# Kernel optimization log

Measured on AMD Instinct MI355X. Metric: run time of the kernel, lower is better.

Reference implementation:

```python
import jax, jax.numpy as jnp
import numpy as np

HEADS = 4
BN_EPS = 1e-5


def _linear_attention(x, heads):
    # x: [B, L, C]; per-head linear attention: softmax(Q,dim=feat) @ (softmax(K,dim=seq)^T @ V)
    B, L, C = x.shape
    dh = C // heads
    h = x.reshape(B, L, heads, dh)
    q = jax.nn.softmax(h, axis=-1)          # softmax over feature dim (dim=2 in torch)
    k = jax.nn.softmax(h, axis=1)           # softmax over sequence dim (dim=1 in torch)
    kv = jnp.einsum('blhd,blhe->bhde', k, h)   # [B, H, dh, dh]
    out = jnp.einsum('blhd,bhde->blhe', q, kv) # [B, L, H, dh]
    return out.reshape(B, L, C)


def setup_inputs() -> dict:
    key = jax.random.key(0)
    ks = jax.random.split(key, 10)
    B, C, L, DOUT, NB = 32, 32, 16384, 10, 3
    s = 0.1
    return {
        'x': jax.random.normal(ks[0], (B, C, L), jnp.float32),
        'fcW1': jax.random.normal(ks[1], (NB, C, C), jnp.float32) * s,
        'fcb1': jax.random.normal(ks[2], (NB, C), jnp.float32) * s,
        'fcW2': jax.random.normal(ks[3], (NB, C, C), jnp.float32) * s,
        'fcb2': jax.random.normal(ks[4], (NB, C), jnp.float32) * s,
        'Wh': jax.random.normal(ks[5], (C, C), jnp.float32) * s,
        'bh': jax.random.normal(ks[6], (C,), jnp.float32) * s,
        'bn_gamma': jnp.ones((C,), jnp.float32),
        'bn_beta': jnp.zeros((C,), jnp.float32),
        'bn_mean': jnp.zeros((C,), jnp.float32),
        'bn_var': jnp.ones((C,), jnp.float32),
        'Wf': jax.random.normal(ks[7], (C, DOUT), jnp.float32) * s,
        'bf': jax.random.normal(ks[8], (DOUT,), jnp.float32) * s,
    }


def reference(x, fcW1, fcb1, fcW2, fcb2, Wh, bh, bn_gamma, bn_beta, bn_mean, bn_var, Wf, bf):
    gelu = lambda t: jax.nn.gelu(t, approximate=False)  # torch default GELU is exact erf
    h = jnp.transpose(x, (0, 2, 1))  # [B, C, L] -> [B, L, C]
    n_blocks = fcW1.shape[0]
    for i in range(n_blocks):
        h = _linear_attention(h, HEADS)
        h = gelu(h @ fcW1[i] + fcb1[i])
        h = gelu(h @ fcW2[i] + fcb2[i])
    pooled = jnp.mean(h, axis=1)  # AdaptiveAvgPool1d(1) over L -> [B, C]
    y = pooled @ Wh + bh
    y = (y - bn_mean) * jax.lax.rsqrt(bn_var + BN_EPS) * bn_gamma + bn_beta  # BatchNorm1d (eval)
    y = gelu(y)
    return y @ Wf + bf
```

## Files before the change

### kernel.cpp

```cpp
#include <hip/hip_runtime.h>
#include <cstddef>

#define B_ 32
#define C_ 32
#define L_ 16384
#define H_ 4
#define DH_ 8
#define NB_ 3
#define DOUT_ 10
#define SEG_ 512
#define S_ (L_/SEG_)

#define TILE 256
#define AST  40
#define OST  260

typedef _Float16 f16_t;
typedef _Float16 f16x2 __attribute__((ext_vector_type(2)));
typedef _Float16 f16x8 __attribute__((ext_vector_type(8)));
typedef float    f32x4 __attribute__((ext_vector_type(4)));

__device__ __forceinline__ float gelu_f(float x){
    const float z  = fabsf(x) * 0.70710678118654752440f;
    const float t  = __builtin_amdgcn_rcpf(fmaf(0.3275911f, z, 1.0f));
    const float e  = __expf(-z * z);
    float p = fmaf(t, 1.061405429f, -1.453152027f);
    p = fmaf(t, p, 1.421413741f);
    p = fmaf(t, p, -0.284496736f);
    p = fmaf(t, p, 0.254829592f);
    const float erfz = 1.0f - p * t * e;
    const float phi  = fmaf(copysignf(erfz, x), 0.5f, 0.5f);
    return x * phi;
}

__global__ __launch_bounds__(256) void stats_kernel(const float* __restrict__ h,
                                                    float* __restrict__ part){
    const int seg = blockIdx.x;
    const int hd  = blockIdx.y;
    const int b   = blockIdx.z;
    const int t   = threadIdx.x;
    const int d   = t >> 5;
    const int j   = t & 31;

    __shared__ float tile[8][SEG_];
    __shared__ float sm[8];

    const float* hb = h + (size_t)b * ((size_t)C_*L_) + (size_t)(hd*DH_)*L_ + (size_t)seg*SEG_;

    for (int f = t; f < 8*SEG_/4; f += 256){
        const int row = f >> 7;
        const int c4  = (f & 127) << 2;
        *(f32x4*)&tile[row][c4] = *(const f32x4*)&hb[(size_t)row*L_ + c4];
    }
    __syncthreads();

    float m = -INFINITY;
    #pragma unroll
    for (int i = 0; i < SEG_/32; i++) m = fmaxf(m, tile[d][j + 32*i]);
    m = fmaxf(m, __shfl_xor(m, 1));
    m = fmaxf(m, __shfl_xor(m, 2));
    m = fmaxf(m, __shfl_xor(m, 4));
    m = fmaxf(m, __shfl_xor(m, 8));
    m = fmaxf(m, __shfl_xor(m, 16));
    if (j == 0) sm[d] = m;
    const float m_d = m;

    float s = 0.0f;
    float kv[8];
    #pragma unroll
    for (int e = 0; e < 8; e++) kv[e] = 0.0f;
    #pragma unroll
    for (int i = 0; i < SEG_/32; i++){
        const int k = j + 32*i;
        const float ek = __expf(tile[d][k] - m_d);
        s += ek;
        #pragma unroll
        for (int e = 0; e < 8; e++) kv[e] = fmaf(ek, tile[e][k], kv[e]);
    }
    s += __shfl_xor(s, 1);  s += __shfl_xor(s, 2);  s += __shfl_xor(s, 4);
    s += __shfl_xor(s, 8);  s += __shfl_xor(s, 16);
    #pragma unroll
    for (int e = 0; e < 8; e++){
        kv[e] += __shfl_xor(kv[e], 1);  kv[e] += __shfl_xor(kv[e], 2);
        kv[e] += __shfl_xor(kv[e], 4);  kv[e] += __shfl_xor(kv[e], 8);
        kv[e] += __shfl_xor(kv[e], 16);
    }
    __syncthreads();

    float* po = part + (size_t)((b*H_ + hd)*S_ + seg) * 80;
    if (j == 0){
        po[8 + d] = s;
        #pragma unroll
        for (int e = 0; e < 8; e++) po[16 + d*8 + e] = kv[e];
    }
    if (t < 8) po[t] = sm[t];
}

__global__ __launch_bounds__(64) void merge_kernel(const float* __restrict__ part,
                                                   float* __restrict__ kvn){
    const int bh = blockIdx.x;
    const int t  = threadIdx.x;
    const int d  = t >> 3;
    const float* p = part + (size_t)bh * S_ * 80;
    float M = -INFINITY;
    for (int s2 = 0; s2 < S_; s2++) M = fmaxf(M, p[s2*80 + d]);
    float ssum = 0.0f, kvsum = 0.0f;
    for (int s2 = 0; s2 < S_; s2++){
        float sc = __expf(p[s2*80 + d] - M);
        ssum  += p[s2*80 + 8  + d] * sc;
        kvsum += p[s2*80 + 16 + t] * sc;
    }
    kvn[(size_t)bh*64 + t] = kvsum / ssum;
}

template<bool LAST>
__global__ __launch_bounds__(256)
__attribute__((amdgpu_waves_per_eu(3, 4)))
void block_kernel(const float* hin,
                  float* hout,
                  const float* __restrict__ kvn,
                  const float* __restrict__ W1,
                  const float* __restrict__ b1,
                  const float* __restrict__ W2,
                  const float* __restrict__ b2,
                  float* __restrict__ pooled){
    __shared__ f16_t Ash[TILE*AST];
    __shared__ f16_t Bsh1[32*AST];
    __shared__ f16_t Bsh2[32*AST];
    __shared__ float sb1[32], sb2[32];
    __shared__ float O16[16*OST];
    __shared__ float pool[32];

    const int tid = threadIdx.x;
    const int b   = blockIdx.y;
    const int l0  = blockIdx.x * TILE;
    const int l   = l0 + tid;
    const size_t base = (size_t)b * ((size_t)C_*L_);
    const float* kv = kvn + (size_t)b * (H_*DH_*DH_);

    for (int i = tid; i < 1024; i += 256){
        const int k = i >> 5, n = i & 31;
        Bsh1[n*AST + k] = (f16_t)W1[i];
        Bsh2[n*AST + k] = (f16_t)W2[i];
    }
    if (tid < 32){ sb1[tid] = b1[tid]; sb2[tid] = b2[tid]; }
    if (LAST && tid < 32) pool[tid] = 0.0f;

    float h[32];
    #pragma unroll
    for (int c = 0; c < 32; c++) h[c] = hin[base + (size_t)c*L_ + l];

    float attn[32];
    #pragma unroll
    for (int hh = 0; hh < 4; hh++){
        float mq = h[hh*8];
        #pragma unroll
        for (int d2 = 1; d2 < 8; d2++) mq = fmaxf(mq, h[hh*8 + d2]);
        float es[8]; float qs = 0.f;
        #pragma unroll
        for (int d2 = 0; d2 < 8; d2++){ es[d2] = __expf(h[hh*8 + d2] - mq); qs += es[d2]; }
        const float inv = __builtin_amdgcn_rcpf(qs);
        #pragma unroll
        for (int e = 0; e < 8; e++){
            float a = 0.f;
            #pragma unroll
            for (int d2 = 0; d2 < 8; d2++) a += es[d2] * kv[hh*64 + d2*8 + e];
            attn[hh*8 + e] = a * inv;
        }
    }

    #pragma unroll
    for (int k2 = 0; k2 < 32; k2 += 2){
        f16x2 pr = { (f16_t)attn[k2], (f16_t)attn[k2+1] };
        *(f16x2*)&Ash[tid*AST + k2] = pr;
    }
    __syncthreads();

    const int wv   = tid >> 6;
    const int lane = tid & 63;
    const int lr   = lane & 15;
    const int lk   = lane >> 4;
    const f32x4 zero = {0.f, 0.f, 0.f, 0.f};

    f16x8 a[4], bw[2];
    f32x4 d[8];

    #pragma unroll
    for (int mt = 0; mt < 4; mt++)
        a[mt] = *(const f16x8*)&Ash[(wv*64 + mt*16 + lr)*AST + lk*8];
    #pragma unroll
    for (int nt = 0; nt < 2; nt++)
        bw[nt] = *(const f16x8*)&Bsh1[(nt*16 + lr)*AST + lk*8];
    #pragma unroll
    for (int nt = 0; nt < 2; nt++)
        #pragma unroll
        for (int mt = 0; mt < 4; mt++)
            d[nt*4+mt] = __builtin_amdgcn_mfma_f32_16x16x32_f16(a[mt], bw[nt], zero, 0, 0, 0);

    #pragma unroll
    for (int nt = 0; nt < 2; nt++){
        const float bias = sb1[nt*16 + lr];
        #pragma unroll
        for (int mt = 0; mt < 4; mt++){
            #pragma unroll
            for (int r = 0; r < 4; r++){
                const float v = gelu_f(d[nt*4+mt][r] + bias);
                Ash[(wv*64 + mt*16 + lk*4 + r)*AST + (nt*16 + lr)] = (f16_t)v;
            }
        }
    }
    __syncthreads();

    #pragma unroll
    for (int mt = 0; mt < 4; mt++)
        a[mt] = *(const f16x8*)&Ash[(wv*64 + mt*16 + lr)*AST + lk*8];
    #pragma unroll
    for (int nt = 0; nt < 2; nt++)
        bw[nt] = *(const f16x8*)&Bsh2[(nt*16 + lr)*AST + lk*8];
    #pragma unroll
    for (int nt = 0; nt < 2; nt++)
        #pragma unroll
        for (int mt = 0; mt < 4; mt++)
            d[nt*4+mt] = __builtin_amdgcn_mfma_f32_16x16x32_f16(a[mt], bw[nt], zero, 0, 0, 0);

    #pragma unroll
    for (int nt = 0; nt < 2; nt++){
        const float bias = sb2[nt*16 + lr];
        #pragma unroll
        for (int mt = 0; mt < 4; mt++)
            #pragma unroll
            for (int r = 0; r < 4; r++)
                d[nt*4+mt][r] = gelu_f(d[nt*4+mt][r] + bias);
    }

    if (!LAST){
        #pragma unroll
        for (int nt = 0; nt < 2; nt++){
            __syncthreads();
            #pragma unroll
            for (int mt = 0; mt < 4; mt++)
                *(f32x4*)&O16[lr*OST + wv*64 + mt*16 + lk*4] = d[nt*4+mt];
            __syncthreads();
            #pragma unroll
            for (int c = 0; c < 16; c++)
                hout[base + (size_t)(nt*16 + c)*L_ + l0 + tid] = O16[c*OST + tid];
        }
    } else {
        __syncthreads();
        #pragma unroll
        for (int nt = 0; nt < 2; nt++){
            float ps = 0.f;
            #pragma unroll
            for (int mt = 0; mt < 4; mt++)
                ps += d[nt*4+mt][0] + d[nt*4+mt][1] + d[nt*4+mt][2] + d[nt*4+mt][3];
            atomicAdd(&pool[nt*16 + lr], ps);
        }
        __syncthreads();
        if (tid < 32) atomicAdd(&pooled[b*32 + tid], pool[tid]);
    }
}

__global__ __launch_bounds__(1024) void head_kernel(const float* __restrict__ pooled,
                                                    const float* __restrict__ Wh,
                                                    const float* __restrict__ bh,
                                                    const float* __restrict__ gam,
                                                    const float* __restrict__ bet,
                                                    const float* __restrict__ mean,
                                                    const float* __restrict__ var,
                                                    const float* __restrict__ Wf,
                                                    const float* __restrict__ bf,
                                                    float* __restrict__ out){
    __shared__ float y2[32][32];
    const int t = threadIdx.x;
    const int b = t >> 5, c = t & 31;
    float a = bh[c];
    const float invL = 1.0f / (float)L_;
    #pragma unroll
    for (int d = 0; d < 32; d++) a += (pooled[b*32 + d] * invL) * Wh[d*32 + c];
    a = (a - mean[c]) * rsqrtf(var[c] + 1e-5f) * gam[c] + bet[c];
    y2[b][c] = gelu_f(a);
    __syncthreads();
    if (t < B_*DOUT_){
        const int b2 = t / DOUT_, j = t % DOUT_;
        float r = bf[j];
        #pragma unroll
        for (int c2 = 0; c2 < 32; c2++) r += y2[b2][c2] * Wf[c2*DOUT_ + j];
        out[t] = r;
    }
}

extern "C" void kernel_launch(void* const* d_in, const int* in_sizes, int n_in,
                              void* d_out, int out_size, void* d_ws, size_t ws_size,
                              hipStream_t stream){
    (void)in_sizes; (void)n_in; (void)out_size; (void)ws_size;
    const float* x    = (const float*)d_in[0];
    const float* fW1  = (const float*)d_in[1];
    const float* fb1  = (const float*)d_in[2];
    const float* fW2  = (const float*)d_in[3];
    const float* fb2  = (const float*)d_in[4];
    const float* Wh   = (const float*)d_in[5];
    const float* bh   = (const float*)d_in[6];
    const float* gam  = (const float*)d_in[7];
    const float* bet  = (const float*)d_in[8];
    const float* mean = (const float*)d_in[9];
    const float* var  = (const float*)d_in[10];
    const float* Wf   = (const float*)d_in[11];
    const float* bf   = (const float*)d_in[12];
    float* out = (float*)d_out;

    float* hbuf   = (float*)d_ws;
    float* part   = hbuf + (size_t)B_*C_*L_;
    float* kvn    = part + (size_t)B_*H_*S_*80;
    float* pooled = kvn  + (size_t)B_*H_*64;

    hipMemsetAsync(pooled, 0, B_*C_*sizeof(float), stream);

    dim3 sgrid(S_, H_, B_);
    dim3 bgrid(L_/TILE, B_);

    stats_kernel<<<sgrid, 256, 0, stream>>>(x, part);
    merge_kernel<<<B_*H_, 64, 0, stream>>>(part, kvn);
    block_kernel<false><<<bgrid, 256, 0, stream>>>(x, hbuf, kvn, fW1, fb1, fW2, fb2, nullptr);
    stats_kernel<<<sgrid, 256, 0, stream>>>(hbuf, part);
    merge_kernel<<<B_*H_, 64, 0, stream>>>(part, kvn);
    block_kernel<false><<<bgrid, 256, 0, stream>>>(hbuf, hbuf, kvn,
        fW1 + C_*C_, fb1 + C_, fW2 + C_*C_, fb2 + C_, nullptr);
    stats_kernel<<<sgrid, 256, 0, stream>>>(hbuf, part);
    merge_kernel<<<B_*H_, 64, 0, stream>>>(part, kvn);
    block_kernel<true><<<bgrid, 256, 0, stream>>>(hbuf, nullptr, kvn,
        fW1 + 2*C_*C_, fb1 + 2*C_, fW2 + 2*C_*C_, fb2 + 2*C_, pooled);

    head_kernel<<<1, 1024, 0, stream>>>(pooled, Wh, bh, gam, bet, mean, var, Wf, bf, out);
}
```

Before: 289.0 us.

## Fuse next-block attention stats into block kernel epilogue and parallelize merge

The block kernel now computes the per-tile softmax max, sum and K^T V partials for the next block while the output tile is still in shared memory. This removes two separate stats_kernel passes that re-read the full activation buffer from global memory. The merge kernel uses 256 threads with a shared-memory reduction over a configurable segment count. Shared memory is reduced by aliasing the A and O staging buffers, and the occupancy hint is raised. The trade-offs are more partial segments to merge, extra register pressure in the epilogue, and a risk of aliasing bugs between the A and O buffers.

After: 311.7 us. 1.08x slower.

```diff
diff --git a/kernel.cpp b/kernel.cpp
--- a/kernel.cpp
+++ b/kernel.cpp
@@ -10,6 +10,7 @@
 #define DOUT_ 10
 #define SEG_ 512
 #define S_ (L_/SEG_)
+#define S2_ (L_/256)
 
 #define TILE 256
 #define AST  40
@@ -33,6 +34,13 @@
     return x * phi;
 }
 
+#define RED_MAX32(v) do{ v = fmaxf(v, __shfl_xor(v,1));  v = fmaxf(v, __shfl_xor(v,2)); \
+                         v = fmaxf(v, __shfl_xor(v,4));  v = fmaxf(v, __shfl_xor(v,8)); \
+                         v = fmaxf(v, __shfl_xor(v,16)); }while(0)
+#define RED_SUM32(v) do{ v += __shfl_xor(v,1);  v += __shfl_xor(v,2); \
+                         v += __shfl_xor(v,4);  v += __shfl_xor(v,8); \
+                         v += __shfl_xor(v,16); }while(0)
+
 __global__ __launch_bounds__(256) void stats_kernel(const float* __restrict__ h,
                                                     float* __restrict__ part){
     const int seg = blockIdx.x;
@@ -57,11 +65,7 @@
     float m = -INFINITY;
     #pragma unroll
     for (int i = 0; i < SEG_/32; i++) m = fmaxf(m, tile[d][j + 32*i]);
-    m = fmaxf(m, __shfl_xor(m, 1));
-    m = fmaxf(m, __shfl_xor(m, 2));
-    m = fmaxf(m, __shfl_xor(m, 4));
-    m = fmaxf(m, __shfl_xor(m, 8));
-    m = fmaxf(m, __shfl_xor(m, 16));
+    RED_MAX32(m);
     if (j == 0) sm[d] = m;
     const float m_d = m;
 
@@ -77,14 +81,9 @@
         #pragma unroll
         for (int e = 0; e < 8; e++) kv[e] = fmaf(ek, tile[e][k], kv[e]);
     }
-    s += __shfl_xor(s, 1);  s += __shfl_xor(s, 2);  s += __shfl_xor(s, 4);
-    s += __shfl_xor(s, 8);  s += __shfl_xor(s, 16);
-    #pragma unroll
-    for (int e = 0; e < 8; e++){
-        kv[e] += __shfl_xor(kv[e], 1);  kv[e] += __shfl_xor(kv[e], 2);
-        kv[e] += __shfl_xor(kv[e], 4);  kv[e] += __shfl_xor(kv[e], 8);
-        kv[e] += __shfl_xor(kv[e], 16);
-    }
+    RED_SUM32(s);
+    #pragma unroll
+    for (int e = 0; e < 8; e++){ RED_SUM32(kv[e]); }
     __syncthreads();
 
     float* po = part + (size_t)((b*H_ + hd)*S_ + seg) * 80;
@@ -96,26 +95,41 @@
     if (t < 8) po[t] = sm[t];
 }
 
-__global__ __launch_bounds__(64) void merge_kernel(const float* __restrict__ part,
-                                                   float* __restrict__ kvn){
+__global__ __launch_bounds__(256) void merge_kernel(const float* __restrict__ part,
+                                                    float* __restrict__ kvn,
+                                                    int nseg){
     const int bh = blockIdx.x;
-    const int t  = threadIdx.x;
+    const int t  = threadIdx.x & 63;
+    const int g  = threadIdx.x >> 6;
     const int d  = t >> 3;
-    const float* p = part + (size_t)bh * S_ * 80;
+    const float* p = part + (size_t)bh * nseg * 80;
+    __shared__ float r1[4][64], r2[4][64];
+
     float M = -INFINITY;
-    for (int s2 = 0; s2 < S_; s2++) M = fmaxf(M, p[s2*80 + d]);
+    for (int s2 = g; s2 < nseg; s2 += 4) M = fmaxf(M, p[s2*80 + d]);
+    r1[g][t] = M;
+    __syncthreads();
+    M = fmaxf(fmaxf(r1[0][t], r1[1][t]), fmaxf(r1[2][t], r1[3][t]));
+    __syncthreads();
+
     float ssum = 0.0f, kvsum = 0.0f;
-    for (int s2 = 0; s2 < S_; s2++){
-        float sc = __expf(p[s2*80 + d] - M);
+    for (int s2 = g; s2 < nseg; s2 += 4){
+        const float sc = __expf(p[s2*80 + d] - M);
         ssum  += p[s2*80 + 8  + d] * sc;
         kvsum += p[s2*80 + 16 + t] * sc;
     }
-    kvn[(size_t)bh*64 + t] = kvsum / ssum;
-}
-
-template<bool LAST>
+    r1[g][t] = ssum; r2[g][t] = kvsum;
+    __syncthreads();
+    if (g == 0){
+        ssum  = r1[0][t]+r1[1][t]+r1[2][t]+r1[3][t];
+        kvsum = r2[0][t]+r2[1][t]+r2[2][t]+r2[3][t];
+        kvn[(size_t)bh*64 + t] = kvsum / ssum;
+    }
+}
+
+template<bool LAST, bool STATS>
 __global__ __launch_bounds__(256)
-__attribute__((amdgpu_waves_per_eu(3, 4)))
+__attribute__((amdgpu_waves_per_eu(6, 8)))
 void block_kernel(const float* hin,
                   float* hout,
                   const float* __restrict__ kvn,
@@ -123,12 +137,14 @@
                   const float* __restrict__ b1,
                   const float* __restrict__ W2,
                   const float* __restrict__ b2,
-                  float* __restrict__ pooled){
-    __shared__ f16_t Ash[TILE*AST];
+                  float* __restrict__ pooled,
+                  float* __restrict__ partout){
+    __shared__ __align__(16) char AObuf[TILE*AST*2];
+    f16_t* const Ash = (f16_t*)AObuf;
+    float* const O16 = (float*)AObuf;
     __shared__ f16_t Bsh1[32*AST];
     __shared__ f16_t Bsh2[32*AST];
     __shared__ float sb1[32], sb2[32];
-    __shared__ float O16[16*OST];
     __shared__ float pool[32];
 
     const int tid = threadIdx.x;
@@ -244,6 +260,43 @@
             #pragma unroll
             for (int c = 0; c < 16; c++)
                 hout[base + (size_t)(nt*16 + c)*L_ + l0 + tid] = O16[c*OST + tid];
+
+            if constexpr (STATS){
+                const int sd = tid >> 5;
+                const int sj = tid & 31;
+                #pragma unroll
+                for (int hh2 = 0; hh2 < 2; hh2++){
+                    const int row = hh2*8 + sd;
+                    float m = -INFINITY;
+                    #pragma unroll
+                    for (int i = 0; i < 8; i++) m = fmaxf(m, O16[row*OST + sj + 32*i]);
+                    RED_MAX32(m);
+                    float s = 0.0f;
+                    float kvp[8];
+                    #pragma unroll
+                    for (int e = 0; e < 8; e++) kvp[e] = 0.0f;
+                    #pragma unroll
+                    for (int i = 0; i < 8; i++){
+                        const int k = sj + 32*i;
+                        const float ek = __expf(O16[row*OST + k] - m);
+                        s += ek;
+                        #pragma unroll
+                        for (int e = 0; e < 8; e++)
+                            kvp[e] = fmaf(ek, O16[(hh2*8+e)*OST + k], kvp[e]);
+                    }
+                    RED_SUM32(s);
+                    #pragma unroll
+                    for (int e = 0; e < 8; e++){ RED_SUM32(kvp[e]); }
+                    if (sj == 0){
+                        float* po = partout +
+                            (size_t)((b*H_ + nt*2 + hh2)*S2_ + blockIdx.x) * 80;
+                        po[sd]     = m;
+                        po[8 + sd] = s;
+                        #pragma unroll
+                        for (int e = 0; e < 8; e++) po[16 + sd*8 + e] = kvp[e];
+                    }
+                }
+            }
         }
     } else {
         __syncthreads();
@@ -310,7 +363,7 @@
 
     float* hbuf   = (float*)d_ws;
     float* part   = hbuf + (size_t)B_*C_*L_;
-    float* kvn    = part + (size_t)B_*H_*S_*80;
+    float* kvn    = part + (size_t)B_*H_*S2_*80;
     float* pooled = kvn  + (size_t)B_*H_*64;
 
     hipMemsetAsync(pooled, 0, B_*C_*sizeof(float), stream);
@@ -319,16 +372,15 @@
     dim3 bgrid(L_/TILE, B_);
 
     stats_kernel<<<sgrid, 256, 0, stream>>>(x, part);
-    merge_kernel<<<B_*H_, 64, 0, stream>>>(part, kvn);
-    block_kernel<false><<<bgrid, 256, 0, stream>>>(x, hbuf, kvn, fW1, fb1, fW2, fb2, nullptr);
-    stats_kernel<<<sgrid, 256, 0, stream>>>(hbuf, part);
-    merge_kernel<<<B_*H_, 64, 0, stream>>>(part, kvn);
-    block_kernel<false><<<bgrid, 256, 0, stream>>>(hbuf, hbuf, kvn,
-        fW1 + C_*C_, fb1 + C_, fW2 + C_*C_, fb2 + C_, nullptr);
-    stats_kernel<<<sgrid, 256, 0, stream>>>(hbuf, part);
-    merge_kernel<<<B_*H_, 64, 0, stream>>>(part, kvn);
-    block_kernel<true><<<bgrid, 256, 0, stream>>>(hbuf, nullptr, kvn,
-        fW1 + 2*C_*C_, fb1 + 2*C_, fW2 + 2*C_*C_, fb2 + 2*C_, pooled);
+    merge_kernel<<<B_*H_, 256, 0, stream>>>(part, kvn, S_);
+    block_kernel<false, true><<<bgrid, 256, 0, stream>>>(x, hbuf, kvn,
+        fW1, fb1, fW2, fb2, nullptr, part);
+    merge_kernel<<<B_*H_, 256, 0, stream>>>(part, kvn, S2_);
+    block_kernel<false, true><<<bgrid, 256, 0, stream>>>(hbuf, hbuf, kvn,
+        fW1 + C_*C_, fb1 + C_, fW2 + C_*C_, fb2 + C_, nullptr, part);
+    merge_kernel<<<B_*H_, 256, 0, stream>>>(part, kvn, S2_);
+    block_kernel<true, false><<<bgrid, 256, 0, stream>>>(hbuf, nullptr, kvn,
+        fW1 + 2*C_*C_, fb1 + 2*C_, fW2 + 2*C_*C_, fb2 + 2*C_, pooled, nullptr);
 
     head_kernel<<<1, 1024, 0, stream>>>(pooled, Wh, bh, gam, bet, mean, var, Wf, bf, out);
 }
```

## Fuse segment-merge into block kernel and alias A/O shared buffers

Applied to the files above, without the earlier changes.

Removes the separate merge kernel: each block now recomputes the per-(batch,head) normalized KV matrix from the per-segment partials directly into shared memory. This eliminates three small kernel launches and the kvn round-trip, at the cost of redundant merge work in every block (64 blocks per batch each read 32 segments of partials). The activation loads are hoisted earlier to overlap with the merge, and the f16 A tile and f32 output staging buffer now share one LDS allocation to cut shared-memory use and potentially raise occupancy.

Measured after the change: 294.1 us. No clear change (+1.7%).

```diff
diff --git a/kernel.cpp b/kernel.cpp
--- a/kernel.cpp
+++ b/kernel.cpp
@@ -33,6 +33,13 @@
     return x * phi;
 }
 
+#define RED_MAX32(v) do{ v = fmaxf(v, __shfl_xor(v,1));  v = fmaxf(v, __shfl_xor(v,2)); \
+                         v = fmaxf(v, __shfl_xor(v,4));  v = fmaxf(v, __shfl_xor(v,8)); \
+                         v = fmaxf(v, __shfl_xor(v,16)); }while(0)
+#define RED_SUM32(v) do{ v += __shfl_xor(v,1);  v += __shfl_xor(v,2); \
+                         v += __shfl_xor(v,4);  v += __shfl_xor(v,8); \
+                         v += __shfl_xor(v,16); }while(0)
+
 __global__ __launch_bounds__(256) void stats_kernel(const float* __restrict__ h,
                                                     float* __restrict__ part){
     const int seg = blockIdx.x;
@@ -57,11 +64,7 @@
     float m = -INFINITY;
     #pragma unroll
     for (int i = 0; i < SEG_/32; i++) m = fmaxf(m, tile[d][j + 32*i]);
-    m = fmaxf(m, __shfl_xor(m, 1));
-    m = fmaxf(m, __shfl_xor(m, 2));
-    m = fmaxf(m, __shfl_xor(m, 4));
-    m = fmaxf(m, __shfl_xor(m, 8));
-    m = fmaxf(m, __shfl_xor(m, 16));
+    RED_MAX32(m);
     if (j == 0) sm[d] = m;
     const float m_d = m;
 
@@ -77,14 +80,9 @@
         #pragma unroll
         for (int e = 0; e < 8; e++) kv[e] = fmaf(ek, tile[e][k], kv[e]);
     }
-    s += __shfl_xor(s, 1);  s += __shfl_xor(s, 2);  s += __shfl_xor(s, 4);
-    s += __shfl_xor(s, 8);  s += __shfl_xor(s, 16);
-    #pragma unroll
-    for (int e = 0; e < 8; e++){
-        kv[e] += __shfl_xor(kv[e], 1);  kv[e] += __shfl_xor(kv[e], 2);
-        kv[e] += __shfl_xor(kv[e], 4);  kv[e] += __shfl_xor(kv[e], 8);
-        kv[e] += __shfl_xor(kv[e], 16);
-    }
+    RED_SUM32(s);
+    #pragma unroll
+    for (int e = 0; e < 8; e++){ RED_SUM32(kv[e]); }
     __syncthreads();
 
     float* po = part + (size_t)((b*H_ + hd)*S_ + seg) * 80;
@@ -94,23 +92,6 @@
         for (int e = 0; e < 8; e++) po[16 + d*8 + e] = kv[e];
     }
     if (t < 8) po[t] = sm[t];
-}
-
-__global__ __launch_bounds__(64) void merge_kernel(const float* __restrict__ part,
-                                                   float* __restrict__ kvn){
-    const int bh = blockIdx.x;
-    const int t  = threadIdx.x;
-    const int d  = t >> 3;
-    const float* p = part + (size_t)bh * S_ * 80;
-    float M = -INFINITY;
-    for (int s2 = 0; s2 < S_; s2++) M = fmaxf(M, p[s2*80 + d]);
-    float ssum = 0.0f, kvsum = 0.0f;
-    for (int s2 = 0; s2 < S_; s2++){
-        float sc = __expf(p[s2*80 + d] - M);
-        ssum  += p[s2*80 + 8  + d] * sc;
-        kvsum += p[s2*80 + 16 + t] * sc;
-    }
-    kvn[(size_t)bh*64 + t] = kvsum / ssum;
 }
 
 template<bool LAST>
@@ -118,17 +99,19 @@
 __attribute__((amdgpu_waves_per_eu(3, 4)))
 void block_kernel(const float* hin,
                   float* hout,
-                  const float* __restrict__ kvn,
+                  const float* __restrict__ part,
                   const float* __restrict__ W1,
                   const float* __restrict__ b1,
                   const float* __restrict__ W2,
                   const float* __restrict__ b2,
                   float* __restrict__ pooled){
-    __shared__ f16_t Ash[TILE*AST];
+    __shared__ __align__(16) char AObuf[TILE*AST*2];
+    f16_t* const Ash = (f16_t*)AObuf;
+    float* const O16 = (float*)AObuf;
     __shared__ f16_t Bsh1[32*AST];
     __shared__ f16_t Bsh2[32*AST];
     __shared__ float sb1[32], sb2[32];
-    __shared__ float O16[16*OST];
+    __shared__ float kvsh[256];
     __shared__ float pool[32];
 
     const int tid = threadIdx.x;
@@ -136,7 +119,10 @@
     const int l0  = blockIdx.x * TILE;
     const int l   = l0 + tid;
     const size_t base = (size_t)b * ((size_t)C_*L_);
-    const float* kv = kvn + (size_t)b * (H_*DH_*DH_);
+
+    float h[32];
+    #pragma unroll
+    for (int c = 0; c < 32; c++) h[c] = hin[base + (size_t)c*L_ + l];
 
     for (int i = tid; i < 1024; i += 256){
         const int k = i >> 5, n = i & 31;
@@ -146,9 +132,22 @@
     if (tid < 32){ sb1[tid] = b1[tid]; sb2[tid] = b2[tid]; }
     if (LAST && tid < 32) pool[tid] = 0.0f;
 
-    float h[32];
-    #pragma unroll
-    for (int c = 0; c < 32; c++) h[c] = hin[base + (size_t)c*L_ + l];
+    {
+        const int hh_t = tid >> 6;
+        const int tt   = tid & 63;
+        const int dd   = tt >> 3;
+        const float* pp = part + (size_t)(b*H_ + hh_t) * S_ * 80;
+        float M = -INFINITY;
+        for (int s2 = 0; s2 < S_; s2++) M = fmaxf(M, pp[s2*80 + dd]);
+        float ssum = 0.0f, kvs = 0.0f;
+        for (int s2 = 0; s2 < S_; s2++){
+            const float sc = __expf(pp[s2*80 + dd] - M);
+            ssum = fmaf(pp[s2*80 + 8  + dd], sc, ssum);
+            kvs  = fmaf(pp[s2*80 + 16 + tt], sc, kvs);
+        }
+        kvsh[tid] = kvs / ssum;
+    }
+    __syncthreads();
 
     float attn[32];
     #pragma unroll
@@ -164,7 +163,7 @@
         for (int e = 0; e < 8; e++){
             float a = 0.f;
             #pragma unroll
-            for (int d2 = 0; d2 < 8; d2++) a += es[d2] * kv[hh*64 + d2*8 + e];
+            for (int d2 = 0; d2 < 8; d2++) a += es[d2] * kvsh[hh*64 + d2*8 + e];
             attn[hh*8 + e] = a * inv;
         }
     }
@@ -310,8 +309,7 @@
 
     float* hbuf   = (float*)d_ws;
     float* part   = hbuf + (size_t)B_*C_*L_;
-    float* kvn    = part + (size_t)B_*H_*S_*80;
-    float* pooled = kvn  + (size_t)B_*H_*64;
+    float* pooled = part + (size_t)B_*H_*S_*80;
 
     hipMemsetAsync(pooled, 0, B_*C_*sizeof(float), stream);
 
@@ -319,15 +317,13 @@
     dim3 bgrid(L_/TILE, B_);
 
     stats_kernel<<<sgrid, 256, 0, stream>>>(x, part);
-    merge_kernel<<<B_*H_, 64, 0, stream>>>(part, kvn);
-    block_kernel<false><<<bgrid, 256, 0, stream>>>(x, hbuf, kvn, fW1, fb1, fW2, fb2, nullptr);
+    block_kernel<false><<<bgrid, 256, 0, stream>>>(x, hbuf, part,
+        fW1, fb1, fW2, fb2, nullptr);
     stats_kernel<<<sgrid, 256, 0, stream>>>(hbuf, part);
-    merge_kernel<<<B_*H_, 64, 0, stream>>>(part, kvn);
-    block_kernel<false><<<bgrid, 256, 0, stream>>>(hbuf, hbuf, kvn,
+    block_kernel<false><<<bgrid, 256, 0, stream>>>(hbuf, hbuf, part,
         fW1 + C_*C_, fb1 + C_, fW2 + C_*C_, fb2 + C_, nullptr);
     stats_kernel<<<sgrid, 256, 0, stream>>>(hbuf, part);
-    merge_kernel<<<B_*H_, 64, 0, stream>>>(part, kvn);
-    block_kernel<true><<<bgrid, 256, 0, stream>>>(hbuf, nullptr, kvn,
+    block_kernel<true><<<bgrid, 256, 0, stream>>>(hbuf, nullptr, part,
         fW1 + 2*C_*C_, fb1 + 2*C_, fW2 + 2*C_*C_, fb2 + 2*C_, pooled);
 
     head_kernel<<<1, 1024, 0, stream>>>(pooled, Wh, bh, gam, bet, mean, var, Wf, bf, out);
```

## Store block outputs directly from MFMA registers and parallelize merge kernel

Applied to the files above, without the earlier changes.

The non-last block kernel now writes MFMA results straight to global memory as 16-byte vector stores. This drops the shared-memory transpose buffer and its barriers, and removes the barrier after the first GELU because each wave only reads back its own rows of Ash. The merge kernel uses 256 threads, with four groups each covering a quarter of the segments, and combines them through shared memory. The activation loads are moved ahead of weight staging so they are issued earlier. The cost is less coalesced stores: each row receives scattered 64-byte chunks instead of full contiguous rows, which may raise write traffic inefficiency, in exchange for lower LDS use and fewer synchronizations.

After: 298.2 us. 3.2% more time.

```diff
diff --git a/kernel.cpp b/kernel.cpp
--- a/kernel.cpp
+++ b/kernel.cpp
@@ -13,7 +13,6 @@
 
 #define TILE 256
 #define AST  40
-#define OST  260
 
 typedef _Float16 f16_t;
 typedef _Float16 f16x2 __attribute__((ext_vector_type(2)));
@@ -33,6 +32,13 @@
     return x * phi;
 }
 
+#define RED_MAX32(v) do{ v = fmaxf(v, __shfl_xor(v,1));  v = fmaxf(v, __shfl_xor(v,2)); \
+                         v = fmaxf(v, __shfl_xor(v,4));  v = fmaxf(v, __shfl_xor(v,8)); \
+                         v = fmaxf(v, __shfl_xor(v,16)); }while(0)
+#define RED_SUM32(v) do{ v += __shfl_xor(v,1);  v += __shfl_xor(v,2); \
+                         v += __shfl_xor(v,4);  v += __shfl_xor(v,8); \
+                         v += __shfl_xor(v,16); }while(0)
+
 __global__ __launch_bounds__(256) void stats_kernel(const float* __restrict__ h,
                                                     float* __restrict__ part){
     const int seg = blockIdx.x;
@@ -57,11 +63,7 @@
     float m = -INFINITY;
     #pragma unroll
     for (int i = 0; i < SEG_/32; i++) m = fmaxf(m, tile[d][j + 32*i]);
-    m = fmaxf(m, __shfl_xor(m, 1));
-    m = fmaxf(m, __shfl_xor(m, 2));
-    m = fmaxf(m, __shfl_xor(m, 4));
-    m = fmaxf(m, __shfl_xor(m, 8));
-    m = fmaxf(m, __shfl_xor(m, 16));
+    RED_MAX32(m);
     if (j == 0) sm[d] = m;
     const float m_d = m;
 
@@ -77,14 +79,9 @@
         #pragma unroll
         for (int e = 0; e < 8; e++) kv[e] = fmaf(ek, tile[e][k], kv[e]);
     }
-    s += __shfl_xor(s, 1);  s += __shfl_xor(s, 2);  s += __shfl_xor(s, 4);
-    s += __shfl_xor(s, 8);  s += __shfl_xor(s, 16);
-    #pragma unroll
-    for (int e = 0; e < 8; e++){
-        kv[e] += __shfl_xor(kv[e], 1);  kv[e] += __shfl_xor(kv[e], 2);
-        kv[e] += __shfl_xor(kv[e], 4);  kv[e] += __shfl_xor(kv[e], 8);
-        kv[e] += __shfl_xor(kv[e], 16);
-    }
+    RED_SUM32(s);
+    #pragma unroll
+    for (int e = 0; e < 8; e++){ RED_SUM32(kv[e]); }
     __syncthreads();
 
     float* po = part + (size_t)((b*H_ + hd)*S_ + seg) * 80;
@@ -96,21 +93,35 @@
     if (t < 8) po[t] = sm[t];
 }
 
-__global__ __launch_bounds__(64) void merge_kernel(const float* __restrict__ part,
-                                                   float* __restrict__ kvn){
+__global__ __launch_bounds__(256) void merge_kernel(const float* __restrict__ part,
+                                                    float* __restrict__ kvn){
     const int bh = blockIdx.x;
-    const int t  = threadIdx.x;
+    const int t  = threadIdx.x & 63;
+    const int g  = threadIdx.x >> 6;
     const int d  = t >> 3;
     const float* p = part + (size_t)bh * S_ * 80;
+    __shared__ float r1[4][64], r2[4][64];
+
     float M = -INFINITY;
-    for (int s2 = 0; s2 < S_; s2++) M = fmaxf(M, p[s2*80 + d]);
+    for (int s2 = g; s2 < S_; s2 += 4) M = fmaxf(M, p[s2*80 + d]);
+    r1[g][t] = M;
+    __syncthreads();
+    M = fmaxf(fmaxf(r1[0][t], r1[1][t]), fmaxf(r1[2][t], r1[3][t]));
+    __syncthreads();
+
     float ssum = 0.0f, kvsum = 0.0f;
-    for (int s2 = 0; s2 < S_; s2++){
-        float sc = __expf(p[s2*80 + d] - M);
+    for (int s2 = g; s2 < S_; s2 += 4){
+        const float sc = __expf(p[s2*80 + d] - M);
         ssum  += p[s2*80 + 8  + d] * sc;
         kvsum += p[s2*80 + 16 + t] * sc;
     }
-    kvn[(size_t)bh*64 + t] = kvsum / ssum;
+    r1[g][t] = ssum; r2[g][t] = kvsum;
+    __syncthreads();
+    if (g == 0){
+        ssum  = r1[0][t]+r1[1][t]+r1[2][t]+r1[3][t];
+        kvsum = r2[0][t]+r2[1][t]+r2[2][t]+r2[3][t];
+        kvn[(size_t)bh*64 + t] = kvsum / ssum;
+    }
 }
 
 template<bool LAST>
@@ -124,11 +135,10 @@
                   const float* __restrict__ W2,
                   const float* __restrict__ b2,
                   float* __restrict__ pooled){
-    __shared__ f16_t Ash[TILE*AST];
+    __shared__ __align__(16) f16_t Ash[TILE*AST];
     __shared__ f16_t Bsh1[32*AST];
     __shared__ f16_t Bsh2[32*AST];
     __shared__ float sb1[32], sb2[32];
-    __shared__ float O16[16*OST];
     __shared__ float pool[32];
 
     const int tid = threadIdx.x;
@@ -138,6 +148,10 @@
     const size_t base = (size_t)b * ((size_t)C_*L_);
     const float* kv = kvn + (size_t)b * (H_*DH_*DH_);
 
+    float h[32];
+    #pragma unroll
+    for (int c = 0; c < 32; c++) h[c] = hin[base + (size_t)c*L_ + l];
+
     for (int i = tid; i < 1024; i += 256){
         const int k = i >> 5, n = i & 31;
         Bsh1[n*AST + k] = (f16_t)W1[i];
@@ -145,10 +159,6 @@
     }
     if (tid < 32){ sb1[tid] = b1[tid]; sb2[tid] = b2[tid]; }
     if (LAST && tid < 32) pool[tid] = 0.0f;
-
-    float h[32];
-    #pragma unroll
-    for (int c = 0; c < 32; c++) h[c] = hin[base + (size_t)c*L_ + l];
 
     float attn[32];
     #pragma unroll
@@ -201,15 +211,13 @@
     for (int nt = 0; nt < 2; nt++){
         const float bias = sb1[nt*16 + lr];
         #pragma unroll
-        for (int mt = 0; mt < 4; mt++){
+        for (int mt = 0; mt < 4; mt++)
             #pragma unroll
             for (int r = 0; r < 4; r++){
                 const float v = gelu_f(d[nt*4+mt][r] + bias);
                 Ash[(wv*64 + mt*16 + lk*4 + r)*AST + (nt*16 + lr)] = (f16_t)v;
             }
-        }
-    }
-    __syncthreads();
+    }
 
     #pragma unroll
     for (int mt = 0; mt < 4; mt++)
@@ -235,18 +243,12 @@
 
     if (!LAST){
         #pragma unroll
-        for (int nt = 0; nt < 2; nt++){
-            __syncthreads();
+        for (int nt = 0; nt < 2; nt++)
             #pragma unroll
             for (int mt = 0; mt < 4; mt++)
-                *(f32x4*)&O16[lr*OST + wv*64 + mt*16 + lk*4] = d[nt*4+mt];
-            __syncthreads();
-            #pragma unroll
-            for (int c = 0; c < 16; c++)
-                hout[base + (size_t)(nt*16 + c)*L_ + l0 + tid] = O16[c*OST + tid];
-        }
+                *(f32x4*)&hout[base + (size_t)(nt*16 + lr)*L_
+                               + l0 + wv*64 + mt*16 + lk*4] = d[nt*4+mt];
     } else {
-        __syncthreads();
         #pragma unroll
         for (int nt = 0; nt < 2; nt++){
             float ps = 0.f;
@@ -319,14 +321,15 @@
     dim3 bgrid(L_/TILE, B_);
 
     stats_kernel<<<sgrid, 256, 0, stream>>>(x, part);
-    merge_kernel<<<B_*H_, 64, 0, stream>>>(part, kvn);
-    block_kernel<false><<<bgrid, 256, 0, stream>>>(x, hbuf, kvn, fW1, fb1, fW2, fb2, nullptr);
+    merge_kernel<<<B_*H_, 256, 0, stream>>>(part, kvn);
+    block_kernel<false><<<bgrid, 256, 0, stream>>>(x, hbuf, kvn,
+        fW1, fb1, fW2, fb2, nullptr);
     stats_kernel<<<sgrid, 256, 0, stream>>>(hbuf, part);
-    merge_kernel<<<B_*H_, 64, 0, stream>>>(part, kvn);
+    merge_kernel<<<B_*H_, 256, 0, stream>>>(part, kvn);
     block_kernel<false><<<bgrid, 256, 0, stream>>>(hbuf, hbuf, kvn,
         fW1 + C_*C_, fb1 + C_, fW2 + C_*C_, fb2 + C_, nullptr);
     stats_kernel<<<sgrid, 256, 0, stream>>>(hbuf, part);
-    merge_kernel<<<B_*H_, 64, 0, stream>>>(part, kvn);
+    merge_kernel<<<B_*H_, 256, 0, stream>>>(part, kvn);
     block_kernel<true><<<bgrid, 256, 0, stream>>>(hbuf, nullptr, kvn,
         fW1 + 2*C_*C_, fb1 + 2*C_, fW2 + 2*C_*C_, fb2 + 2*C_, pooled);
 
```
